# Kernel tuning notes

Measured on AMD Instinct MI355X. Metric: run time of the kernel, lower is better.

## Reference

```python
import jax, jax.numpy as jnp
import numpy as np

EPS = 1e-06

def setup_inputs() -> dict:
    key = jax.random.key(0)
    k1, k2, k3, k4 = jax.random.split(key, 4)
    N, E, D = 100000, 1600000, 128
    feat = jax.random.normal(k1, (N, D), dtype=jnp.float32)
    src = jax.random.randint(k2, (E,), 0, N, dtype=jnp.int32)
    dst = jax.random.randint(k3, (E,), 0, N, dtype=jnp.int32)
    W = jax.random.normal(k4, (D, D), dtype=jnp.float32) * 0.05
    b = jnp.zeros((D,), dtype=jnp.float32)
    a2 = jnp.ones((D,), dtype=jnp.float32)
    b2 = jnp.zeros((D,), dtype=jnp.float32)
    return {"feat": feat, "src": src, "dst": dst, "W": W, "b": b, "a2": a2, "b2": b2}

def reference(feat, src, dst, W, b, a2, b2):
    N, D = feat.shape
    # LayerNorm (torch std is unbiased, eps added to std, not var)
    mean = jnp.mean(feat, axis=-1, keepdims=True)
    std = jnp.std(feat, axis=-1, keepdims=True, ddof=1)
    h = a2 * (feat - mean) / (std + EPS) + b2
    # DGL GraphConv, norm='both': D_out^{-1/2} gather-sum D_in^{-1/2}, then W, b, relu
    ones = jnp.ones(src.shape[0], dtype=feat.dtype)
    out_deg = jax.ops.segment_sum(ones, src, num_segments=N)
    in_deg = jax.ops.segment_sum(ones, dst, num_segments=N)
    norm_out = jax.lax.rsqrt(jnp.maximum(out_deg, 1.0))[:, None]
    norm_in = jax.lax.rsqrt(jnp.maximum(in_deg, 1.0))[:, None]
    h = h * norm_out
    # in_feats == out_feats -> DGL multiplies weight first
    h = h @ W
    agg = jax.ops.segment_sum(h[src], dst, num_segments=N)  # [N, D]
    rst = agg * norm_in + b
    rst = jax.nn.relu(rst)
    # residual (Identity since in_feats == out_feats); dropout is identity at eval
    return rst + feat
```

## Files before the change

### kernel.cpp

```cpp
#include <hip/hip_runtime.h>

#define D 128
#define BSH 6
#define BN 64
#define NBUK_MAX 2048
#define NBLK 256
#define SRT_CAP 2048
#define NW_LDS 25600

typedef __bf16 bf16x8 __attribute__((ext_vector_type(8)));
typedef float  f32x4  __attribute__((ext_vector_type(4)));

__device__ __forceinline__ unsigned short f2bf(float f) {
    unsigned u = __float_as_uint(f);
    unsigned r = (u + 0x7FFF + ((u >> 16) & 1)) >> 16;
    return (unsigned short)r;
}
__device__ __forceinline__ float bf2f(unsigned short s) {
    return __uint_as_float(((unsigned)s) << 16);
}

__global__ __launch_bounds__(1024) void count_kernel(const int* __restrict__ src,
        const int* __restrict__ dst, int* __restrict__ hist,
        unsigned* __restrict__ partial, int E, int nbuk, int chunk, int NW) {
    __shared__ unsigned ph[NW_LDS];
    __shared__ int hb[NBUK_MAX];
    int t = threadIdx.x;
    for (int i = t; i < NW_LDS; i += 1024) ph[i] = 0;
    for (int i = t; i < nbuk; i += 1024) hb[i] = 0;
    __syncthreads();
    int lo = blockIdx.x * chunk;
    int hi = min(E, lo + chunk);
    for (int e = lo + t; e < hi; e += 1024) {
        int s = src[e], d = dst[e];
        atomicAdd(&ph[s >> 2], 1u << ((s & 3) * 8));
        atomicAdd(&hb[d >> BSH], 1);
    }
    __syncthreads();
    int* hrow = hist + (size_t)blockIdx.x * nbuk;
    for (int i = t; i < nbuk; i += 1024) hrow[i] = hb[i];
    unsigned* prow = partial + (size_t)blockIdx.x * NW;
    for (int i = t; i < NW; i += 1024) prow[i] = ph[i];
}

__global__ __launch_bounds__(1024) void reduce_kernel(const unsigned* __restrict__ partial,
        unsigned* __restrict__ podeg, int NW) {
    __shared__ unsigned acc[16][64];
    int t = threadIdx.x;
    int wl = t & 63, bg = t >> 6;
    int w = blockIdx.x * 64 + wl;
    unsigned s = 0;
    if (w < NW) {
        for (int b = bg; b < NBLK; b += 16) s += partial[(size_t)b * NW + w];
    }
    acc[bg][wl] = s;
    __syncthreads();
    if (bg == 0 && w < NW) {
        unsigned tot = 0;
        #pragma unroll
        for (int g = 0; g < 16; ++g) tot += acc[g][wl];
        podeg[w] = tot;
    }
}

__global__ __launch_bounds__(64) void hscan_kernel(int* __restrict__ hist,
        int* __restrict__ colsum, int nbuk) {
    int buk = blockIdx.x;
    int l = threadIdx.x;
    int v[4]; int s = 0;
    #pragma unroll
    for (int i = 0; i < 4; ++i) {
        v[i] = hist[(size_t)(l * 4 + i) * nbuk + buk];
        s += v[i];
    }
    int x = s;
    #pragma unroll
    for (int m = 1; m < 64; m <<= 1) {
        int y = __shfl_up(x, m);
        if (l >= m) x += y;
    }
    int base = x - s;
    #pragma unroll
    for (int i = 0; i < 4; ++i) {
        int tmp = v[i];
        hist[(size_t)(l * 4 + i) * nbuk + buk] = base;
        base += tmp;
    }
    if (l == 63) colsum[buk] = x;
}

__global__ __launch_bounds__(1024) void bscan_kernel(const int* __restrict__ colsum,
        int* __restrict__ base, int nbuk, int E) {
    __shared__ int s[1024];
    int t = threadIdx.x;
    int i0 = 2 * t, i1 = 2 * t + 1;
    int a = (i0 < nbuk) ? colsum[i0] : 0;
    int c = (i1 < nbuk) ? colsum[i1] : 0;
    int p = a + c;
    s[t] = p;
    __syncthreads();
    #pragma unroll
    for (int off = 1; off < 1024; off <<= 1) {
        int x = (t >= off) ? s[t - off] : 0;
        __syncthreads();
        s[t] += x;
        __syncthreads();
    }
    int ex = s[t] - p;
    if (i0 < nbuk) base[i0] = ex;
    if (i1 < nbuk) base[i1] = ex + a;
    if (t == 0) base[nbuk] = E;
}

__global__ __launch_bounds__(1024) void scatter_kernel(const int* __restrict__ src,
        const int* __restrict__ dst, const int* __restrict__ hist,
        const int* __restrict__ base, unsigned* __restrict__ pairs,
        int E, int nbuk, int chunk) {
    __shared__ int cur[NBUK_MAX];
    int t = threadIdx.x;
    const int* hrow = hist + (size_t)blockIdx.x * nbuk;
    for (int i = t; i < nbuk; i += 1024) cur[i] = base[i] + hrow[i];
    __syncthreads();
    int lo = blockIdx.x * chunk;
    int hi = min(E, lo + chunk);
    for (int e = lo + t; e < hi; e += 1024) {
        int d = dst[e];
        int pos = atomicAdd(&cur[d >> BSH], 1);
        pairs[pos] = ((unsigned)(d & (BN - 1)) << 24) | (unsigned)src[e];
    }
}

__global__ __launch_bounds__(256) void ln_gemm_kernel(const float* __restrict__ feat,
        const float* __restrict__ W, const float* __restrict__ a2, const float* __restrict__ b2,
        const unsigned* __restrict__ podeg, unsigned short* __restrict__ hw, int N) {
    __shared__ unsigned short Wt[D * D];
    __shared__ unsigned short hs[64 * D];

    const int t = threadIdx.x;
    const int base = blockIdx.x * 64;

    {
        const float4* W4 = (const float4*)W;
        #pragma unroll
        for (int i = 0; i < 16; ++i) {
            int idx = i * 256 + t;
            int k = idx >> 5;
            int c0 = (idx & 31) * 4;
            float4 wv = W4[idx];
            Wt[(c0 + 0) * D + (k ^ (((c0 + 0) & 7) << 3))] = f2bf(wv.x);
            Wt[(c0 + 1) * D + (k ^ (((c0 + 1) & 7) << 3))] = f2bf(wv.y);
            Wt[(c0 + 2) * D + (k ^ (((c0 + 2) & 7) << 3))] = f2bf(wv.z);
            Wt[(c0 + 3) * D + (k ^ (((c0 + 3) & 7) << 3))] = f2bf(wv.w);
        }
    }

    {
        const int r = t >> 2;
        const int sub = t & 3;
        const int grow = base + r;
        const bool valid = grow < N;

        float4 v[8];
        float sum = 0.f, sumsq = 0.f;
        if (valid) {
            const float4* fr = (const float4*)(feat + (size_t)grow * D + sub * 32);
            #pragma unroll
            for (int i = 0; i < 8; ++i) {
                v[i] = fr[i];
                sum   += v[i].x + v[i].y + v[i].z + v[i].w;
                sumsq += v[i].x * v[i].x + v[i].y * v[i].y + v[i].z * v[i].z + v[i].w * v[i].w;
            }
        }
        sum   += __shfl_xor(sum, 1);   sumsq += __shfl_xor(sumsq, 1);
        sum   += __shfl_xor(sum, 2);   sumsq += __shfl_xor(sumsq, 2);

        if (valid) {
            float mean = sum * (1.f / 128.f);
            float var  = fmaxf((sumsq - 128.f * mean * mean) * (1.f / 127.f), 0.f);
            float inv  = 1.f / (sqrtf(var) + 1e-6f);
            int   od   = (podeg[grow >> 2] >> ((grow & 3) * 8)) & 0xFF;
            float norm = rsqrtf(fmaxf((float)od, 1.f));
            float sa   = inv * norm;
            #pragma unroll
            for (int i = 0; i < 8; ++i) {
                int c0 = sub * 32 + i * 4;
                float4 av = *(const float4*)&a2[c0];
                float4 bv = *(const float4*)&b2[c0];
                ushort4 o;
                o.x = f2bf(av.x * (v[i].x - mean) * sa + bv.x * norm);
                o.y = f2bf(av.y * (v[i].y - mean) * sa + bv.y * norm);
                o.z = f2bf(av.z * (v[i].z - mean) * sa + bv.z * norm);
                o.w = f2bf(av.w * (v[i].w - mean) * sa + bv.w * norm);
                *(ushort4*)&hs[r * D + (c0 ^ ((r & 7) << 3))] = o;
            }
        } else {
            ushort4 z = make_ushort4(0, 0, 0, 0);
            #pragma unroll
            for (int i = 0; i < 8; ++i) {
                int c0 = sub * 32 + i * 4;
                *(ushort4*)&hs[r * D + (c0 ^ ((r & 7) << 3))] = z;
            }
        }
    }
    __syncthreads();

    {
        const int w = t >> 6;
        const int l = t & 63;
        const int lrow = l & 15;
        const int kg = l >> 4;
        const int arow = w * 16 + lrow;

        bf16x8 a[4];
        #pragma unroll
        for (int kt = 0; kt < 4; ++kt) {
            int col = kt * 32 + kg * 8;
            a[kt] = *reinterpret_cast<const bf16x8*>(&hs[arow * D + (col ^ ((arow & 7) << 3))]);
        }

        f32x4 acc[8];
        #pragma unroll
        for (int ct = 0; ct < 8; ++ct) acc[ct] = (f32x4){0.f, 0.f, 0.f, 0.f};

        #pragma unroll
        for (int ct = 0; ct < 8; ++ct) {
            int brow = ct * 16 + lrow;
            #pragma unroll
            for (int kt = 0; kt < 4; ++kt) {
                int col = kt * 32 + kg * 8;
                bf16x8 bfr = *reinterpret_cast<const bf16x8*>(&Wt[brow * D + (col ^ ((brow & 7) << 3))]);
                acc[ct] = __builtin_amdgcn_mfma_f32_16x16x32_bf16(a[kt], bfr, acc[ct], 0, 0, 0);
            }
        }

        #pragma unroll
        for (int ct = 0; ct < 8; ++ct) {
            #pragma unroll
            for (int p = 0; p < 4; ++p) {
                int gr = base + w * 16 + kg * 4 + p;
                if (gr < N) hw[(size_t)gr * D + ct * 16 + lrow] = f2bf(acc[ct][p]);
            }
        }
    }
}

__global__ __launch_bounds__(512) void gather_kernel(const unsigned* __restrict__ pairs,
        const int* __restrict__ bukbase, const unsigned short* __restrict__ hw,
        const float* __restrict__ feat, const float* __restrict__ bias,
        float* __restrict__ out, int N) {
    __shared__ unsigned srt[SRT_CAP];
    __shared__ int cnt[BN];
    __shared__ int ofs[BN + 1];

    int t = threadIdx.x;
    int buk = blockIdx.x;
    int beg = bukbase[buk];
    int ne = bukbase[buk + 1] - beg;
    if (ne > SRT_CAP) ne = SRT_CAP;

    if (t < BN) cnt[t] = 0;
    __syncthreads();

    for (int i = t; i < ne; i += 512)
        atomicAdd(&cnt[pairs[beg + i] >> 24], 1);
    __syncthreads();

    if (t < BN) {
        int c = cnt[t];
        int x = c;
        #pragma unroll
        for (int m = 1; m < BN; m <<= 1) {
            int y = __shfl_up(x, m);
            if (t >= m) x += y;
        }
        ofs[t] = x - c;
        if (t == BN - 1) ofs[BN] = x;
        cnt[t] = x - c;
    }
    __syncthreads();

    for (int i = t; i < ne; i += 512) {
        unsigned p = pairs[beg + i];
        int pos = atomicAdd(&cnt[p >> 24], 1);
        srt[pos] = p & 0xFFFFFFu;
    }
    __syncthreads();

    int wv = t >> 6;
    int lane = t & 63;
    int co = lane * 2;

    for (int nl = wv; nl < BN; nl += 8) {
        int n = (buk << BSH) + nl;
        if (n >= N) break;
        int s0 = ofs[nl], s1 = ofs[nl + 1];
        int deg = s1 - s0;

        float a0 = 0.f, a1 = 0.f;
        int e = s0;
        for (; e + 3 < s1; e += 4) {
            int x0 = srt[e], x1 = srt[e + 1], x2 = srt[e + 2], x3 = srt[e + 3];
            ushort2 q0 = *(const ushort2*)&hw[(size_t)x0 * D + co];
            ushort2 q1 = *(const ushort2*)&hw[(size_t)x1 * D + co];
            ushort2 q2 = *(const ushort2*)&hw[(size_t)x2 * D + co];
            ushort2 q3 = *(const ushort2*)&hw[(size_t)x3 * D + co];
            a0 += bf2f(q0.x) + bf2f(q1.x) + bf2f(q2.x) + bf2f(q3.x);
            a1 += bf2f(q0.y) + bf2f(q1.y) + bf2f(q2.y) + bf2f(q3.y);
        }
        for (; e < s1; ++e) {
            int x0 = srt[e];
            ushort2 q0 = *(const ushort2*)&hw[(size_t)x0 * D + co];
            a0 += bf2f(q0.x);
            a1 += bf2f(q0.y);
        }

        float ni = rsqrtf(fmaxf((float)deg, 1.f));
        float2 bb = *(const float2*)&bias[co];
        float2 f  = *(const float2*)&feat[(size_t)n * D + co];
        float2 o;
        o.x = fmaxf(fmaf(a0, ni, bb.x), 0.f) + f.x;
        o.y = fmaxf(fmaf(a1, ni, bb.y), 0.f) + f.y;
        *(float2*)&out[(size_t)n * D + co] = o;
    }
}

extern "C" void kernel_launch(void* const* d_in, const int* in_sizes, int n_in,
                              void* d_out, int out_size, void* d_ws, size_t ws_size,
                              hipStream_t stream) {
    const float* feat = (const float*)d_in[0];
    const int*   src  = (const int*)d_in[1];
    const int*   dst  = (const int*)d_in[2];
    const float* W    = (const float*)d_in[3];
    const float* b    = (const float*)d_in[4];
    const float* a2   = (const float*)d_in[5];
    const float* b2   = (const float*)d_in[6];

    const int N = in_sizes[0] / D;
    const int E = in_sizes[1];
    const int NW = (N + 3) / 4;
    const int nbuk = (N + BN - 1) >> BSH;
    const int chunk = (E + NBLK - 1) / NBLK;

    float* out = (float*)d_out;

    unsigned short* hw = (unsigned short*)d_ws;
    unsigned* podeg = (unsigned*)(hw + (size_t)N * D);
    int* hist    = (int*)(podeg + NW);
    int* colsum  = hist + (size_t)NBLK * NBUK_MAX;
    int* bukbase = colsum + NBUK_MAX;
    unsigned* pairs = (unsigned*)(bukbase + (NBUK_MAX + 1));
    unsigned* partial = pairs + E;

    count_kernel<<<NBLK, 1024, 0, stream>>>(src, dst, hist, partial, E, nbuk, chunk, NW);
    reduce_kernel<<<(NW + 63) / 64, 1024, 0, stream>>>(partial, podeg, NW);
    hscan_kernel<<<nbuk, 64, 0, stream>>>(hist, colsum, nbuk);
    bscan_kernel<<<1, 1024, 0, stream>>>(colsum, bukbase, nbuk, E);
    scatter_kernel<<<NBLK, 1024, 0, stream>>>(src, dst, hist, bukbase, pairs, E, nbuk, chunk);

    ln_gemm_kernel<<<(N + 63) / 64, 256, 0, stream>>>(feat, W, a2, b2, podeg, hw, N);

    gather_kernel<<<nbuk, 512, 0, stream>>>(pairs, bukbase, hw, feat, b, out, N);
}
```

Baseline: 158.7 us.

## Pre-pack bf16 weights once and widen gather loads to 8 bytes with split edges

A new small kernel converts W to swizzled bf16 once, so each ln_gemm block copies packed 16-byte chunks into LDS instead of converting the fp32 weights with scattered 2-byte stores in every block. The gather kernel now has each half-wavefront handle alternating edges with ushort4 (8-byte) loads covering 4 columns. The two partial sums are combined with a cross-half shuffle. This aims to cut per-block weight conversion overhead and issue fewer, wider gather loads, at the cost of an extra launch and idle lanes in the epilogue.

```diff
diff --git a/kernel.cpp b/kernel.cpp
--- a/kernel.cpp
+++ b/kernel.cpp
@@ -18,6 +18,14 @@
 }
 __device__ __forceinline__ float bf2f(unsigned short s) {
     return __uint_as_float(((unsigned)s) << 16);
+}
+
+__global__ __launch_bounds__(256) void wpack_kernel(const float* __restrict__ W,
+        unsigned short* __restrict__ Wp) {
+    int idx = blockIdx.x * 256 + threadIdx.x;
+    int k = idx >> 7;
+    int c = idx & 127;
+    Wp[c * D + (k ^ ((c & 7) << 3))] = f2bf(W[idx]);
 }
 
 __global__ __launch_bounds__(1024) void count_kernel(const int* __restrict__ src,
@@ -131,8 +139,9 @@
 }
 
 __global__ __launch_bounds__(256) void ln_gemm_kernel(const float* __restrict__ feat,
-        const float* __restrict__ W, const float* __restrict__ a2, const float* __restrict__ b2,
-        const unsigned* __restrict__ podeg, unsigned short* __restrict__ hw, int N) {
+        const unsigned short* __restrict__ Wp, const float* __restrict__ a2,
+        const float* __restrict__ b2, const unsigned* __restrict__ podeg,
+        unsigned short* __restrict__ hw, int N) {
     __shared__ unsigned short Wt[D * D];
     __shared__ unsigned short hs[64 * D];
 
@@ -140,18 +149,10 @@
     const int base = blockIdx.x * 64;
 
     {
-        const float4* W4 = (const float4*)W;
-        #pragma unroll
-        for (int i = 0; i < 16; ++i) {
-            int idx = i * 256 + t;
-            int k = idx >> 5;
-            int c0 = (idx & 31) * 4;
-            float4 wv = W4[idx];
-            Wt[(c0 + 0) * D + (k ^ (((c0 + 0) & 7) << 3))] = f2bf(wv.x);
-            Wt[(c0 + 1) * D + (k ^ (((c0 + 1) & 7) << 3))] = f2bf(wv.y);
-            Wt[(c0 + 2) * D + (k ^ (((c0 + 2) & 7) << 3))] = f2bf(wv.z);
-            Wt[(c0 + 3) * D + (k ^ (((c0 + 3) & 7) << 3))] = f2bf(wv.w);
-        }
+        const uint4* Wp4 = (const uint4*)Wp;
+        uint4* Wl4 = (uint4*)Wt;
+        #pragma unroll
+        for (int i = 0; i < 8; ++i) Wl4[i * 256 + t] = Wp4[i * 256 + t];
     }
 
     {
@@ -288,7 +289,9 @@
 
     int wv = t >> 6;
     int lane = t & 63;
-    int co = lane * 2;
+    int half = lane >> 5;
+    int l32 = lane & 31;
+    int co = l32 * 4;
 
     for (int nl = wv; nl < BN; nl += 8) {
         int n = (buk << BSH) + nl;
@@ -296,31 +299,44 @@
         int s0 = ofs[nl], s1 = ofs[nl + 1];
         int deg = s1 - s0;
 
-        float a0 = 0.f, a1 = 0.f;
-        int e = s0;
-        for (; e + 3 < s1; e += 4) {
-            int x0 = srt[e], x1 = srt[e + 1], x2 = srt[e + 2], x3 = srt[e + 3];
-            ushort2 q0 = *(const ushort2*)&hw[(size_t)x0 * D + co];
-            ushort2 q1 = *(const ushort2*)&hw[(size_t)x1 * D + co];
-            ushort2 q2 = *(const ushort2*)&hw[(size_t)x2 * D + co];
-            ushort2 q3 = *(const ushort2*)&hw[(size_t)x3 * D + co];
-            a0 += bf2f(q0.x) + bf2f(q1.x) + bf2f(q2.x) + bf2f(q3.x);
-            a1 += bf2f(q0.y) + bf2f(q1.y) + bf2f(q2.y) + bf2f(q3.y);
-        }
-        for (; e < s1; ++e) {
+        float a0 = 0.f, a1 = 0.f, a2v = 0.f, a3 = 0.f;
+        int e = s0 + half;
+        for (; e + 6 < s1; e += 8) {
+            int x0 = srt[e], x1 = srt[e + 2], x2 = srt[e + 4], x3 = srt[e + 6];
+            ushort4 q0 = *(const ushort4*)&hw[(size_t)x0 * D + co];
+            ushort4 q1 = *(const ushort4*)&hw[(size_t)x1 * D + co];
+            ushort4 q2 = *(const ushort4*)&hw[(size_t)x2 * D + co];
+            ushort4 q3 = *(const ushort4*)&hw[(size_t)x3 * D + co];
+            a0  += bf2f(q0.x) + bf2f(q1.x) + bf2f(q2.x) + bf2f(q3.x);
+            a1  += bf2f(q0.y) + bf2f(q1.y) + bf2f(q2.y) + bf2f(q3.y);
+            a2v += bf2f(q0.z) + bf2f(q1.z) + bf2f(q2.z) + bf2f(q3.z);
+            a3  += bf2f(q0.w) + bf2f(q1.w) + bf2f(q2.w) + bf2f(q3.w);
+        }
+        for (; e < s1; e += 2) {
             int x0 = srt[e];
-            ushort2 q0 = *(const ushort2*)&hw[(size_t)x0 * D + co];
-            a0 += bf2f(q0.x);
-            a1 += bf2f(q0.y);
-        }
-
-        float ni = rsqrtf(fmaxf((float)deg, 1.f));
-        float2 bb = *(const float2*)&bias[co];
-        float2 f  = *(const float2*)&feat[(size_t)n * D + co];
-        float2 o;
-        o.x = fmaxf(fmaf(a0, ni, bb.x), 0.f) + f.x;
-        o.y = fmaxf(fmaf(a1, ni, bb.y), 0.f) + f.y;
-        *(float2*)&out[(size_t)n * D + co] = o;
+            ushort4 q0 = *(const ushort4*)&hw[(size_t)x0 * D + co];
+            a0  += bf2f(q0.x);
+            a1  += bf2f(q0.y);
+            a2v += bf2f(q0.z);
+            a3  += bf2f(q0.w);
+        }
+
+        a0  += __shfl_xor(a0, 32);
+        a1  += __shfl_xor(a1, 32);
+        a2v += __shfl_xor(a2v, 32);
+        a3  += __shfl_xor(a3, 32);
+
+        if (half == 0) {
+            float ni = rsqrtf(fmaxf((float)deg, 1.f));
+            float4 bb = *(const float4*)&bias[co];
+            float4 f  = *(const float4*)&feat[(size_t)n * D + co];
+            float4 o;
+            o.x = fmaxf(fmaf(a0,  ni, bb.x), 0.f) + f.x;
+            o.y = fmaxf(fmaf(a1,  ni, bb.y), 0.f) + f.y;
+            o.z = fmaxf(fmaf(a2v, ni, bb.z), 0.f) + f.z;
+            o.w = fmaxf(fmaf(a3,  ni, bb.w), 0.f) + f.w;
+            *(float4*)&out[(size_t)n * D + co] = o;
+        }
     }
 }
 
@@ -348,16 +364,18 @@
     int* hist    = (int*)(podeg + NW);
     int* colsum  = hist + (size_t)NBLK * NBUK_MAX;
     int* bukbase = colsum + NBUK_MAX;
-    unsigned* pairs = (unsigned*)(bukbase + (NBUK_MAX + 1));
+    unsigned short* Wp = (unsigned short*)(bukbase + (NBUK_MAX + 1));
+    unsigned* pairs = (unsigned*)(Wp + D * D);
     unsigned* partial = pairs + E;
 
+    wpack_kernel<<<64, 256, 0, stream>>>(W, Wp);
     count_kernel<<<NBLK, 1024, 0, stream>>>(src, dst, hist, partial, E, nbuk, chunk, NW);
     reduce_kernel<<<(NW + 63) / 64, 1024, 0, stream>>>(partial, podeg, NW);
     hscan_kernel<<<nbuk, 64, 0, stream>>>(hist, colsum, nbuk);
     bscan_kernel<<<1, 1024, 0, stream>>>(colsum, bukbase, nbuk, E);
     scatter_kernel<<<NBLK, 1024, 0, stream>>>(src, dst, hist, bukbase, pairs, E, nbuk, chunk);
 
-    ln_gemm_kernel<<<(N + 63) / 64, 256, 0, stream>>>(feat, W, a2, b2, podeg, hw, N);
+    ln_gemm_kernel<<<(N + 63) / 64, 256, 0, stream>>>(feat, Wp, a2, b2, podeg, hw, N);
 
     gather_kernel<<<nbuk, 512, 0, stream>>>(pairs, bukbase, hw, feat, b, out, N);
 }
```

Measured after the change: 151.8 us. 1.04x faster.
